# Kernel optimization log

Hardware: AMD Instinct MI355X
Metric: run time of the kernel (lower is better)

The kernel has to match this reference:

```python
import jax, jax.numpy as jnp
import numpy as np

N1, N2, P, D = 8, 8, 1024, 768  # 8 query / 8 normal images, 32x32 patches, ViT-B dim
PH = PW = 32
H = W = 512


def setup_inputs() -> dict:
    key = jax.random.key(0)
    k1, k2 = jax.random.split(key)
    feats = jax.random.normal(k1, (N1, P, D), dtype=jnp.float32)
    nfeats = jax.random.normal(k2, (N2, P, D), dtype=jnp.float32)
    return {"feats": feats, "nfeats": nfeats, "ph": PH, "pw": PW, "h": H, "w": W}


def _bilinear_resize(x, out_h, out_w):
    # x: [N, h, w] -> [N, out_h, out_w]; matches F.interpolate(mode='bilinear', align_corners=False)
    n, h, w = x.shape
    sy = (jnp.arange(out_h, dtype=x.dtype) + 0.5) * (h / out_h) - 0.5
    sx = (jnp.arange(out_w, dtype=x.dtype) + 0.5) * (w / out_w) - 0.5
    y0f = jnp.floor(sy)
    x0f = jnp.floor(sx)
    wy = (sy - y0f)[None, :, None]  # [1, out_h, 1]
    wx = (sx - x0f)[None, None, :]  # [1, 1, out_w]
    y0 = jnp.clip(y0f.astype(jnp.int32), 0, h - 1)
    y1 = jnp.clip(y0f.astype(jnp.int32) + 1, 0, h - 1)
    x0 = jnp.clip(x0f.astype(jnp.int32), 0, w - 1)
    x1 = jnp.clip(x0f.astype(jnp.int32) + 1, 0, w - 1)
    v00 = x[:, y0[:, None], x0[None, :]]
    v01 = x[:, y0[:, None], x1[None, :]]
    v10 = x[:, y1[:, None], x0[None, :]]
    v11 = x[:, y1[:, None], x1[None, :]]
    top = v00 * (1 - wx) + v01 * wx
    bot = v10 * (1 - wx) + v11 * wx
    return top * (1 - wy) + bot * wy


def reference(feats, nfeats, ph, pw, h, w):
    # L2-normalize patch embeddings (as in forward: f / f.norm(dim=-1, keepdim=True))
    f = feats / jnp.linalg.norm(feats, axis=-1, keepdims=True)   # [N1, P, D]
    g = nfeats / jnp.linalg.norm(nfeats, axis=-1, keepdims=True)  # [N2, P, D]
    n1 = f.shape[0]
    # cdist(feats.reshape(N1*P,D), nfeats.reshape(N2*P,D)).reshape(N1,P,N2,P).permute(0,2,1,3)
    gram = jnp.einsum('npd,mqd->nmpq', f, g)                      # [N1, N2, P, P]
    fa2 = jnp.sum(f * f, axis=-1)                                 # [N1, P]
    gb2 = jnp.sum(g * g, axis=-1)                                 # [N2, P]
    d2 = fa2[:, None, :, None] + gb2[None, :, None, :] - 2.0 * gram
    dist = jnp.sqrt(jnp.maximum(d2, 0.0)) * 0.5                   # distances / 2
    # nearest-normal-patch distance per query patch (bg mask is all ones here)
    scores_patch = jnp.min(dist, axis=-1)                         # [N1, N2, P]
    scores = jnp.mean(jnp.max(scores_patch, axis=-1), axis=1)     # [N1]
    sp = jnp.mean(scores_patch, axis=1).reshape(n1, ph, pw)       # [N1, PH, PW]
    scores_pixel = _bilinear_resize(sp, h, w)                     # [N1, H, W]
    return scores, scores_pixel
```

## Files before the change

kernel.cpp:

```cpp
#include <hip/hip_runtime.h>
#include <hip/hip_bf16.h>
#include <stdint.h>

#define N1 8
#define N2 8
#define PP 1024
#define DD 768
#define PH 32
#define PW 32
#define OH 512
#define OW 512

#define NKT 12

typedef int i32x4 __attribute__((ext_vector_type(4)));

__global__ __launch_bounds__(256) void nrm_kernel(
    const float* __restrict__ inA, const float* __restrict__ inB,
    char* __restrict__ outA, char* __restrict__ outB) {
  int row = blockIdx.x;
  const float* src;
  char* dst;
  if (row < N1 * PP) {
    src = inA + (size_t)row * DD;
    dst = outA + (size_t)row * DD;
  } else {
    row -= N1 * PP;
    src = inB + (size_t)row * DD;
    dst = outB + (size_t)row * DD;
  }
  const int t = threadIdx.x;
  const float v0 = src[t], v1 = src[t + 256], v2 = src[t + 512];
  float s = v0 * v0 + v1 * v1 + v2 * v2;
#pragma unroll
  for (int m = 32; m; m >>= 1) s += __shfl_xor(s, m, 64);
  __shared__ float red[4];
  const int wave = t >> 6, lane = t & 63;
  if (lane == 0) red[wave] = s;
  __syncthreads();
  const float inv = 127.0f / sqrtf(red[0] + red[1] + red[2] + red[3]);
  dst[t]       = (char)__float2int_rn(v0 * inv);
  dst[t + 256] = (char)__float2int_rn(v1 * inv);
  dst[t + 512] = (char)__float2int_rn(v2 * inv);
}

__device__ __forceinline__ void gll16(const char* src, char* dst) {
  __builtin_amdgcn_global_load_lds(
      (const __attribute__((address_space(1))) void*)src,
      (__attribute__((address_space(3))) void*)dst, 16, 0, 0);
}

__global__ __launch_bounds__(256, 4) void grami8_kernel(
    const char* __restrict__ fq, const char* __restrict__ gq,
    int* __restrict__ rowmaxI) {
  __shared__ __align__(16) char lds[2][2][8192];

  const int bid = blockIdx.x;
  const int wg = (bid & 7) * 512 + (bid >> 3);
  const int pair = wg >> 6;
  const int tile = wg & 63;
  const int fn = pair >> 3, gm = pair & 7;
  const int mt = tile >> 3, nt = tile & 7;
  const int brow = mt * 128, bcol = nt * 128;

  const int t = threadIdx.x;
  const int lane = t & 63, wave = t >> 6;
  const int lr = lane & 15, lk = lane >> 4;
  const int wr = wave >> 1, wc = wave & 1;

  const char* rowA = fq + ((size_t)fn * PP + brow) * DD;
  const char* rowB = gq + ((size_t)gm * PP + bcol) * DD;

  int srow[2], scol[2];
#pragma unroll
  for (int j = 0; j < 2; ++j) {
    const int c = t + j * 256;
    const int x = (c * 16) ^ (((c >> 3) & 7) << 4);
    srow[j] = x >> 6;
    scol[j] = x & 63;
  }

  const int swzv = ((lr >> 1) & 7) << 4;
  const int abase = ((wr * 64 + lr) * 64 + lk * 16) ^ swzv;
  const int bbase = ((wc * 64 + lr) * 64 + lk * 16) ^ swzv;

#define STAGE(rowPtr, kt, slot, mat)                                      \
  do {                                                                    \
    _Pragma("unroll")                                                     \
    for (int j = 0; j < 2; ++j)                                           \
      gll16(rowPtr + (size_t)srow[j] * DD + (kt) * 64 + scol[j],          \
            &lds[slot][mat][(t + j * 256) * 16]);                         \
  } while (0)

  i32x4 acc[4][4];
#pragma unroll
  for (int i = 0; i < 4; ++i)
#pragma unroll
    for (int j = 0; j < 4; ++j) acc[i][j] = (i32x4){0, 0, 0, 0};

  STAGE(rowB, 0, 0, 1);
  STAGE(rowA, 0, 0, 0);
  asm volatile("s_waitcnt vmcnt(0)" ::: "memory");
  __builtin_amdgcn_s_barrier();
  asm volatile("" ::: "memory");

#pragma unroll 1
  for (int k = 0; k < NKT; ++k) {
    const char* Ab = &lds[k & 1][0][0];
    const char* Bb = &lds[k & 1][1][0];

    if (k + 1 < NKT) {
      const int ns = (k + 1) & 1;
      STAGE(rowB, k + 1, ns, 1);
      STAGE(rowA, k + 1, ns, 0);
    }

    i32x4 a[4], b[4];
#pragma unroll
    for (int n = 0; n < 4; ++n)
      b[n] = *(const i32x4*)(Bb + bbase + n * 1024);
#pragma unroll
    for (int m = 0; m < 4; ++m)
      a[m] = *(const i32x4*)(Ab + abase + m * 1024);

#pragma unroll
    for (int m = 0; m < 4; ++m)
#pragma unroll
      for (int n = 0; n < 4; ++n)
        acc[m][n] = __builtin_amdgcn_mfma_i32_16x16x64_i8(a[m], b[n],
                                                          acc[m][n], 0, 0, 0);

    asm volatile("s_waitcnt vmcnt(0)" ::: "memory");
    __builtin_amdgcn_s_barrier();
    asm volatile("" ::: "memory");
  }

  int* rm = rowmaxI + (size_t)(fn * 8 + gm) * PP;
#pragma unroll
  for (int m = 0; m < 4; ++m) {
#pragma unroll
    for (int r = 0; r < 4; ++r) {
      int vv = max(max(acc[m][0][r], acc[m][1][r]),
                   max(acc[m][2][r], acc[m][3][r]));
      vv = max(vv, __shfl_xor(vv, 1, 64));
      vv = max(vv, __shfl_xor(vv, 2, 64));
      vv = max(vv, __shfl_xor(vv, 4, 64));
      vv = max(vv, __shfl_xor(vv, 8, 64));
      if (lr == 0) {
        const int row = brow + wr * 64 + m * 16 + lk * 4 + r;
        atomicMax(&rm[row], vv);
      }
    }
  }
#undef STAGE
}

__global__ __launch_bounds__(256) void finalize_kernel(
    const int* __restrict__ rowmaxI, float* __restrict__ sp,
    float* __restrict__ scores) {
  const int n = blockIdx.x, t = threadIdx.x;
  const int lane = t & 63, wave = t >> 6;
  __shared__ float red[4];
  __shared__ float maxd[N2];
  float spacc[4] = {0.f, 0.f, 0.f, 0.f};
  for (int m = 0; m < N2; ++m) {
    float lmax = -1e30f;
#pragma unroll
    for (int i = 0; i < 4; ++i) {
      const int p = t + i * 256;
      const float g = (float)rowmaxI[(size_t)(n * N2 + m) * PP + p] *
                      (1.0f / 16129.0f);
      const float d = 0.5f * sqrtf(fmaxf(0.f, 2.f - 2.f * g));
      spacc[i] += d;
      lmax = fmaxf(lmax, d);
    }
#pragma unroll
    for (int msk = 32; msk; msk >>= 1) lmax = fmaxf(lmax, __shfl_xor(lmax, msk, 64));
    if (lane == 0) red[wave] = lmax;
    __syncthreads();
    if (t == 0) maxd[m] = fmaxf(fmaxf(red[0], red[1]), fmaxf(red[2], red[3]));
    __syncthreads();
  }
  if (t == 0) {
    float s = 0.f;
    for (int m = 0; m < N2; ++m) s += maxd[m];
    scores[n] = s * (1.0f / N2);
  }
#pragma unroll
  for (int i = 0; i < 4; ++i)
    sp[(size_t)n * PP + t + i * 256] = spacc[i] * (1.0f / N2);
}

__global__ __launch_bounds__(256) void resize_kernel(
    const float* __restrict__ sp, float* __restrict__ out) {
  const int idx = blockIdx.x * 256 + threadIdx.x;
  const int ox = idx & (OW - 1);
  const int oy = (idx >> 9) & (OH - 1);
  const int n = idx >> 18;
  const float sy = (oy + 0.5f) * ((float)PH / OH) - 0.5f;
  const float sx = (ox + 0.5f) * ((float)PW / OW) - 0.5f;
  const float y0f = floorf(sy), x0f = floorf(sx);
  const float wy = sy - y0f, wx = sx - x0f;
  int y0 = (int)y0f, x0 = (int)x0f;
  int y1 = y0 + 1, x1 = x0 + 1;
  y0 = min(max(y0, 0), PH - 1);
  y1 = min(max(y1, 0), PH - 1);
  x0 = min(max(x0, 0), PW - 1);
  x1 = min(max(x1, 0), PW - 1);
  const float* s = sp + (size_t)n * PP;
  const float v00 = s[y0 * PW + x0], v01 = s[y0 * PW + x1];
  const float v10 = s[y1 * PW + x0], v11 = s[y1 * PW + x1];
  const float top = v00 * (1.f - wx) + v01 * wx;
  const float bot = v10 * (1.f - wx) + v11 * wx;
  out[idx] = top * (1.f - wy) + bot * wy;
}

extern "C" void kernel_launch(void* const* d_in, const int* in_sizes, int n_in,
                              void* d_out, int out_size, void* d_ws, size_t ws_size,
                              hipStream_t stream) {
  const float* feats = (const float*)d_in[0];
  const float* nfeats = (const float*)d_in[1];
  float* out = (float*)d_out;

  char* ws = (char*)d_ws;
  const size_t FQ_BYTES = (size_t)N1 * PP * DD;
  char* fq = ws;
  char* gq = ws + FQ_BYTES;
  int* rowmaxI = (int*)(ws + 2 * FQ_BYTES);
  float* sp = (float*)(ws + 2 * FQ_BYTES + (size_t)N1 * N2 * PP * 4);

  hipMemsetAsync(rowmaxI, 0x80, (size_t)N1 * N2 * PP * 4, stream);

  nrm_kernel<<<(N1 + N2) * PP, 256, 0, stream>>>(feats, nfeats, fq, gq);

  grami8_kernel<<<4096, 256, 0, stream>>>(fq, gq, rowmaxI);

  finalize_kernel<<<N1, 256, 0, stream>>>(rowmaxI, sp, out);
  resize_kernel<<<(N1 * OH * OW) / 256, 256, 0, stream>>>(sp, out + 8);
}
```

Baseline: 115.9 us.

## Keep full A row-block resident in LDS and stream B tiles per workgroup

The gram kernel now gives each 512-thread workgroup a full 128-row A block (all K) held in LDS in MFMA-fragment packed order. It then loops over four 256-column B tiles, double-buffering B and folding the row max in registers. The per-row max is reduced in LDS and written directly, which removes the global atomics and the memset. This cuts redundant A reloads and launch count, but shrinks the grid from 4096 to 512 blocks with large LDS use. That lowers occupancy and may leave CUs underused, and the packed layout has no swizzle, so LDS bank conflicts are possible.

Result: slower. 127.3 us (+9.9%).

```diff
diff --git a/kernel.cpp b/kernel.cpp
--- a/kernel.cpp
+++ b/kernel.cpp
@@ -12,6 +12,8 @@
 #define OW 512
 
 #define NKT 12
+#define NNT 4
+#define NIT (NKT * NNT)
 
 typedef int i32x4 __attribute__((ext_vector_type(4)));
 
@@ -50,46 +52,53 @@
       (__attribute__((address_space(3))) void*)dst, 16, 0, 0);
 }
 
-__global__ __launch_bounds__(256, 4) void grami8_kernel(
+__global__ __launch_bounds__(512) void grami8_kernel(
     const char* __restrict__ fq, const char* __restrict__ gq,
     int* __restrict__ rowmaxI) {
-  __shared__ __align__(16) char lds[2][2][8192];
+  __shared__ __align__(16) char Apk[8 * 12 * 1024];
+  __shared__ __align__(16) char Bpk[2][16 * 1024];
+  __shared__ int rred[128];
 
   const int bid = blockIdx.x;
-  const int wg = (bid & 7) * 512 + (bid >> 3);
-  const int pair = wg >> 6;
-  const int tile = wg & 63;
+  const int wg = (bid & 7) * 64 + (bid >> 3);
+  const int pair = wg >> 3;
+  const int mt = wg & 7;
   const int fn = pair >> 3, gm = pair & 7;
-  const int mt = tile >> 3, nt = tile & 7;
-  const int brow = mt * 128, bcol = nt * 128;
+  const int brow = mt * 128;
 
   const int t = threadIdx.x;
   const int lane = t & 63, wave = t >> 6;
   const int lr = lane & 15, lk = lane >> 4;
-  const int wr = wave >> 1, wc = wave & 1;
+  const int wr = wave >> 2, wc = wave & 3;
 
   const char* rowA = fq + ((size_t)fn * PP + brow) * DD;
-  const char* rowB = gq + ((size_t)gm * PP + bcol) * DD;
-
-  int srow[2], scol[2];
-#pragma unroll
-  for (int j = 0; j < 2; ++j) {
-    const int c = t + j * 256;
-    const int x = (c * 16) ^ (((c >> 3) & 7) << 4);
-    srow[j] = x >> 6;
-    scol[j] = x & 63;
-  }
-
-  const int swzv = ((lr >> 1) & 7) << 4;
-  const int abase = ((wr * 64 + lr) * 64 + lk * 16) ^ swzv;
-  const int bbase = ((wc * 64 + lr) * 64 + lk * 16) ^ swzv;
-
-#define STAGE(rowPtr, kt, slot, mat)                                      \
-  do {                                                                    \
-    _Pragma("unroll")                                                     \
-    for (int j = 0; j < 2; ++j)                                           \
-      gll16(rowPtr + (size_t)srow[j] * DD + (kt) * 64 + scol[j],          \
-            &lds[slot][mat][(t + j * 256) * 16]);                         \
+  const char* rowB = gq + (size_t)gm * PP * DD;
+
+  if (t < 128) rred[t] = (int)0x80000000;
+
+#pragma unroll
+  for (int j = 0; j < 12; ++j) {
+    const int c = t + j * 512;
+    const int rowblk = c / 768;
+    const int rem = c - rowblk * 768;
+    const int kt = rem >> 6;
+    const int ln = rem & 63;
+    gll16(rowA + (size_t)(rowblk * 16 + (ln & 15)) * DD + kt * 64 + (ln >> 4) * 16,
+          &Apk[c * 16]);
+  }
+
+#define STAGE_B(it)                                                          \
+  do {                                                                       \
+    const int nt_ = (it) / NKT, kt_ = (it) - nt_ * NKT;                      \
+    const int slot_ = (it) & 1;                                              \
+    _Pragma("unroll")                                                        \
+    for (int j = 0; j < 2; ++j) {                                            \
+      const int c2 = t + j * 512;                                            \
+      const int colblk = c2 >> 6, ln = c2 & 63;                              \
+      gll16(rowB + (size_t)(nt_ * 256 + colblk * 16 + (ln & 15)) * DD +      \
+                kt_ * 64 + (ln >> 4) * 16,                                   \
+            &Bpk[slot_][c2 * 16]);                                           \
+    }                                                                        \
   } while (0)
 
   i32x4 acc[4][4];
@@ -97,31 +106,31 @@
   for (int i = 0; i < 4; ++i)
 #pragma unroll
     for (int j = 0; j < 4; ++j) acc[i][j] = (i32x4){0, 0, 0, 0};
-
-  STAGE(rowB, 0, 0, 1);
-  STAGE(rowA, 0, 0, 0);
+  int rmax[4][4];
+#pragma unroll
+  for (int i = 0; i < 4; ++i)
+#pragma unroll
+    for (int j = 0; j < 4; ++j) rmax[i][j] = (int)0x80000000;
+
+  STAGE_B(0);
   asm volatile("s_waitcnt vmcnt(0)" ::: "memory");
   __builtin_amdgcn_s_barrier();
   asm volatile("" ::: "memory");
 
 #pragma unroll 1
-  for (int k = 0; k < NKT; ++k) {
-    const char* Ab = &lds[k & 1][0][0];
-    const char* Bb = &lds[k & 1][1][0];
-
-    if (k + 1 < NKT) {
-      const int ns = (k + 1) & 1;
-      STAGE(rowB, k + 1, ns, 1);
-      STAGE(rowA, k + 1, ns, 0);
-    }
+  for (int it = 0; it < NIT; ++it) {
+    const int kt = it % NKT;
+    const char* Bb = &Bpk[it & 1][0];
+
+    if (it + 1 < NIT) STAGE_B(it + 1);
 
     i32x4 a[4], b[4];
 #pragma unroll
+    for (int m = 0; m < 4; ++m)
+      a[m] = *(const i32x4*)(&Apk[(((wr * 4 + m) * NKT + kt) * 64 + lane) * 16]);
+#pragma unroll
     for (int n = 0; n < 4; ++n)
-      b[n] = *(const i32x4*)(Bb + bbase + n * 1024);
-#pragma unroll
-    for (int m = 0; m < 4; ++m)
-      a[m] = *(const i32x4*)(Ab + abase + m * 1024);
+      b[n] = *(const i32x4*)(Bb + ((wc * 4 + n) * 64 + lane) * 16);
 
 #pragma unroll
     for (int m = 0; m < 4; ++m)
@@ -130,29 +139,44 @@
         acc[m][n] = __builtin_amdgcn_mfma_i32_16x16x64_i8(a[m], b[n],
                                                           acc[m][n], 0, 0, 0);
 
+    if (kt == NKT - 1) {
+#pragma unroll
+      for (int m = 0; m < 4; ++m) {
+#pragma unroll
+        for (int r = 0; r < 4; ++r) {
+          const int vv = max(max(acc[m][0][r], acc[m][1][r]),
+                             max(acc[m][2][r], acc[m][3][r]));
+          rmax[m][r] = max(rmax[m][r], vv);
+        }
+#pragma unroll
+        for (int n = 0; n < 4; ++n) acc[m][n] = (i32x4){0, 0, 0, 0};
+      }
+    }
+
     asm volatile("s_waitcnt vmcnt(0)" ::: "memory");
     __builtin_amdgcn_s_barrier();
     asm volatile("" ::: "memory");
   }
 
-  int* rm = rowmaxI + (size_t)(fn * 8 + gm) * PP;
 #pragma unroll
   for (int m = 0; m < 4; ++m) {
 #pragma unroll
     for (int r = 0; r < 4; ++r) {
-      int vv = max(max(acc[m][0][r], acc[m][1][r]),
-                   max(acc[m][2][r], acc[m][3][r]));
+      int vv = rmax[m][r];
       vv = max(vv, __shfl_xor(vv, 1, 64));
       vv = max(vv, __shfl_xor(vv, 2, 64));
       vv = max(vv, __shfl_xor(vv, 4, 64));
       vv = max(vv, __shfl_xor(vv, 8, 64));
       if (lr == 0) {
-        const int row = brow + wr * 64 + m * 16 + lk * 4 + r;
-        atomicMax(&rm[row], vv);
+        atomicMax(&rred[wr * 64 + m * 16 + lk * 4 + r], vv);
       }
     }
   }
-#undef STAGE
+  __syncthreads();
+  if (t < 128) {
+    rowmaxI[(size_t)pair * PP + brow + t] = rred[t];
+  }
+#undef STAGE_B
 }
 
 __global__ __launch_bounds__(256) void finalize_kernel(
@@ -229,11 +253,10 @@
   int* rowmaxI = (int*)(ws + 2 * FQ_BYTES);
   float* sp = (float*)(ws + 2 * FQ_BYTES + (size_t)N1 * N2 * PP * 4);
 
-  hipMemsetAsync(rowmaxI, 0x80, (size_t)N1 * N2 * PP * 4, stream);
 
   nrm_kernel<<<(N1 + N2) * PP, 256, 0, stream>>>(feats, nfeats, fq, gq);
 
-  grami8_kernel<<<4096, 256, 0, stream>>>(fq, gq, rowmaxI);
+  grami8_kernel<<<512, 512, 0, stream>>>(fq, gq, rowmaxI);
 
   finalize_kernel<<<N1, 256, 0, stream>>>(rowmaxI, sp, out);
   resize_kernel<<<(N1 * OH * OW) / 256, 256, 0, stream>>>(sp, out + 8);
```
